# Kernel tuning notes

Hardware: AMD Instinct MI355X
Metric: run time of the kernel (lower is better)

Reference implementation:

```python
import jax, jax.numpy as jnp
import numpy as np

NUM_ITERATIONS = 3


def squash(s):
    # Faithful to the torch code: norm taken over dim=2 of (B,1,out_units,out_size,1),
    # i.e. over the out_units axis of (B, out_units, out_size).
    mag_sq = jnp.sum(s * s, axis=1, keepdims=True)  # (B,1,out_size)
    mag = jnp.sqrt(mag_sq)
    return mag_sq / (1.0 + mag_sq) * (s / mag)


def setup_inputs() -> dict:
    key = jax.random.key(0)
    k1, k2 = jax.random.split(key)
    B, in_units, in_size = 256, 8, 1152
    out_units, out_size = 10, 16
    x = jax.random.normal(k1, (B, in_units, in_size), dtype=jnp.float32)
    W = jax.random.normal(k2, (1, in_size, out_units, out_size, in_units), dtype=jnp.float32)
    return {"x": x, "W": W}


def reference(x, W):
    B = x.shape[0]
    in_size, out_units, out_size, in_units = W.shape[1:]
    Wm = W[0]  # (in_size, out_units, out_size, in_units)
    # u_hat[b,i,j,d] = sum_u W[i,j,d,u] * x[b,u,i]
    u_hat = jnp.einsum("ijdu,bui->bijd", Wm, x)  # (B, in_size, out_units, out_size)

    b_ij = jnp.ones((in_size, out_units), dtype=x.dtype)
    v = None
    for _ in range(NUM_ITERATIONS):
        c_ij = jax.nn.softmax(b_ij, axis=0)  # softmax over in_size (dim=1 in torch)
        s_j = jnp.einsum("ij,bijd->bjd", c_ij, u_hat)  # (B, out_units, out_size)
        v = squash(s_j)
        # agreement, averaged over batch as in the torch code
        u_vj1 = jnp.einsum("bijd,bjd->ij", u_hat, v) / B
        b_ij = b_ij + u_vj1
    # torch returns v_j.squeeze(1) with trailing singleton: (B, out_units, out_size, 1)
    return v[..., None]
```

## Files before the change

### kernel.cpp

```cpp
#include <hip/hip_runtime.h>
#include <cstddef>

#define BB   256
#define UU   8
#define ISZ  1152
#define JJ   10
#define DD   16
#define JD   (JJ*DD)
#define K1   (UU*ISZ)
#define ICH  16
#define NIC  (ISZ/ICH)
#define NJH  5

typedef short v8s __attribute__((ext_vector_type(8)));
typedef float f4v __attribute__((ext_vector_type(4)));
typedef unsigned short ush;

__device__ __forceinline__ ush f2bf(float f) {
    unsigned int u = __float_as_uint(f);
    unsigned int r = (u + 0x7fffu + ((u >> 16) & 1u)) >> 16;
    return (ush)r;
}
__device__ __forceinline__ float bf2f(ush h) {
    return __uint_as_float(((unsigned int)h) << 16);
}

__global__ void prep_kernel(const float* __restrict__ x,
                            ush* __restrict__ xsh, ush* __restrict__ xsl,
                            ush* __restrict__ xth, ush* __restrict__ xtl,
                            float* __restrict__ b_ij) {
    __shared__ float buf[32][8][65];
    int it = blockIdx.x;
    int bt = blockIdx.y;
    int i0 = it * 64, b0 = bt * 32;
    int t = threadIdx.x, lane = t & 63, wv = t >> 6;

    int flat = bt * 18 + it;
    if (flat < 45) b_ij[flat * 256 + t] = 1.0f;

    for (int rep = 0; rep < 64; ++rep) {
        int row = rep * 4 + wv;
        int bl = row >> 3, u = row & 7;
        buf[bl][u][lane] = x[(size_t)(b0 + bl) * K1 + (size_t)u * ISZ + i0 + lane];
    }
    __syncthreads();
    {
        int bl = t >> 3, u = t & 7;
        for (int il = 0; il < 64; ++il) {
            float v = buf[bl][u][il];
            ush h = f2bf(v);
            size_t o = (size_t)(i0 + il) * 2048 + (size_t)(b0 + bl) * 8 + u;
            xsh[o] = h; xsl[o] = f2bf(v - bf2f(h));
        }
    }
    {
        int g = t >> 5, bl = t & 31;
        for (int pass = 0; pass < 64; ++pass) {
            int cu = pass * 8 + g;
            int u = cu >> 6, il = cu & 63;
            float v = buf[bl][u][il];
            ush h = f2bf(v);
            size_t o = (size_t)(u * ISZ + i0 + il) * BB + b0 + bl;
            xth[o] = h; xtl[o] = f2bf(v - bf2f(h));
        }
    }
}

__global__ __launch_bounds__(256, 2) void sgemm_fused(
        const ush* __restrict__ xsh, const ush* __restrict__ xsl,
        const float* __restrict__ W, const float* __restrict__ b_ij,
        float* __restrict__ s_part, int first) {
    int jh = blockIdx.x, ic = blockIdx.y;
    int j0 = jh * 2, i0 = ic * ICH;
    int t = threadIdx.x, lane = t & 63, wv = t >> 6;
    int col = lane & 15, q = lane >> 4;

    __shared__ __align__(16) ush bh_[2][16][136];
    __shared__ __align__(16) ush bl_[2][16][136];
    __shared__ float c_lds[2][ICH];
    __shared__ float redm[4], reds[4];

    if (first) {
        if (t < 2 * ICH) c_lds[t >> 4][t & 15] = 1.0f / 1152.0f;
    } else {
        for (int jj = 0; jj < 2; ++jj) {
            const float* bp = b_ij + (size_t)(j0 + jj) * ISZ;
            float m = -1e30f;
            for (int k = t; k < ISZ; k += 256) m = fmaxf(m, bp[k]);
#pragma unroll
            for (int off = 32; off; off >>= 1) m = fmaxf(m, __shfl_down(m, off, 64));
            if (lane == 0) redm[wv] = m;
            __syncthreads();
            m = fmaxf(fmaxf(redm[0], redm[1]), fmaxf(redm[2], redm[3]));
            float ss = 0.f;
            for (int k = t; k < ISZ; k += 256) ss += __expf(bp[k] - m);
#pragma unroll
            for (int off = 32; off; off >>= 1) ss += __shfl_down(ss, off, 64);
            if (lane == 0) reds[wv] = ss;
            __syncthreads();
            float inv = 1.f / (reds[0] + reds[1] + reds[2] + reds[3]);
            if (t < ICH) c_lds[jj][t] = __expf(bp[i0 + t] - m) * inv;
            __syncthreads();
        }
    }
    __syncthreads();

    for (int slot = t; slot < 512; slot += 256) {
        int jj = slot >> 8, rem = slot & 255, ii = rem >> 4, d = rem & 15;
        const float* wp = W + (size_t)(i0 + ii) * 1280 + (j0 + jj) * 128 + d * 8;
        float4 wa = *(const float4*)wp;
        float4 wb = *(const float4*)(wp + 4);
        float ci = c_lds[jj][ii];
        float vals[8] = { wa.x * ci, wa.y * ci, wa.z * ci, wa.w * ci,
                          wb.x * ci, wb.y * ci, wb.z * ci, wb.w * ci };
        v8s hv, lv;
#pragma unroll
        for (int u = 0; u < 8; ++u) {
            ush h = f2bf(vals[u]);
            hv[u] = (short)h;
            lv[u] = (short)f2bf(vals[u] - bf2f(h));
        }
        *(v8s*)&bh_[jj][d][ii * 8] = hv;
        *(v8s*)&bl_[jj][d][ii * 8] = lv;
    }
    __syncthreads();

    int m_base = wv * 64;
    f4v acc[4][2];
#pragma unroll
    for (int mm = 0; mm < 4; ++mm)
#pragma unroll
        for (int jj = 0; jj < 2; ++jj) acc[mm][jj] = (f4v){0.f, 0.f, 0.f, 0.f};

#pragma unroll
    for (int s = 0; s < 4; ++s) {
        v8s bh0 = *(const v8s*)&bh_[0][col][s * 32 + q * 8];
        v8s bl0 = *(const v8s*)&bl_[0][col][s * 32 + q * 8];
        v8s bh1 = *(const v8s*)&bh_[1][col][s * 32 + q * 8];
        v8s bl1 = *(const v8s*)&bl_[1][col][s * 32 + q * 8];
        size_t abase = (size_t)(i0 + s * 4 + q) * 2048;
#pragma unroll
        for (int mm = 0; mm < 4; ++mm) {
            size_t ao = abase + (size_t)(m_base + mm * 16 + col) * 8;
            v8s ah = *(const v8s*)(xsh + ao);
            v8s al = *(const v8s*)(xsl + ao);
            acc[mm][0] = __builtin_amdgcn_mfma_f32_16x16x32_bf16(ah, bh0, acc[mm][0], 0, 0, 0);
            acc[mm][0] = __builtin_amdgcn_mfma_f32_16x16x32_bf16(ah, bl0, acc[mm][0], 0, 0, 0);
            acc[mm][0] = __builtin_amdgcn_mfma_f32_16x16x32_bf16(al, bh0, acc[mm][0], 0, 0, 0);
            acc[mm][1] = __builtin_amdgcn_mfma_f32_16x16x32_bf16(ah, bh1, acc[mm][1], 0, 0, 0);
            acc[mm][1] = __builtin_amdgcn_mfma_f32_16x16x32_bf16(ah, bl1, acc[mm][1], 0, 0, 0);
            acc[mm][1] = __builtin_amdgcn_mfma_f32_16x16x32_bf16(al, bh1, acc[mm][1], 0, 0, 0);
        }
    }
#pragma unroll
    for (int mm = 0; mm < 4; ++mm)
#pragma unroll
        for (int jj = 0; jj < 2; ++jj)
#pragma unroll
            for (int r = 0; r < 4; ++r)
                s_part[((size_t)ic * BB + m_base + mm * 16 + q * 4 + r) * JD
                       + (j0 + jj) * DD + col] = acc[mm][jj][r];
}

__global__ void reduce_squash(const float* __restrict__ s_part, float* __restrict__ v,
                              ush* __restrict__ vth, ush* __restrict__ vtl) {
    int b = blockIdx.x, t = threadIdx.x;
    __shared__ float sm[JD];
    if (t < JD) {
        float s = 0.f;
#pragma unroll 8
        for (int p = 0; p < NIC; ++p) s += s_part[((size_t)p * BB + b) * JD + t];
        sm[t] = s;
    }
    __syncthreads();
    if (t < JD) {
        int d = t & 15;
        float msq = 0.f;
#pragma unroll
        for (int j = 0; j < JJ; ++j) { float xx = sm[j * DD + d]; msq += xx * xx; }
        float val = msq / (1.f + msq) * sm[t] * rsqrtf(msq);
        v[(size_t)b * JD + t] = val;
        ush h = f2bf(val);
        vth[(size_t)t * BB + b] = h;
        vtl[(size_t)t * BB + b] = f2bf(val - bf2f(h));
    }
}

__global__ __launch_bounds__(256) void mgemm_agree(
        const ush* __restrict__ Ah, const ush* __restrict__ Al,
        const ush* __restrict__ Bh, const ush* __restrict__ Bl,
        const float* __restrict__ W, float* __restrict__ b_ij) {
    int w = threadIdx.x >> 6, lane = threadIdx.x & 63;
    int wj = blockIdx.x * 4 + w;
    int mt = wj / 576, nt = wj % 576;
    int m0 = mt * 16, n0 = nt * 16;
    int col = lane & 15, q = lane >> 4;
    size_t aoff = (size_t)(m0 + col) * BB + q * 8;
    size_t boff = (size_t)(n0 + col) * BB + q * 8;
    f4v acc = {0.f, 0.f, 0.f, 0.f};
#pragma unroll
    for (int s = 0; s < BB / 32; ++s) {
        v8s ah = *(const v8s*)(Ah + aoff);
        v8s al = *(const v8s*)(Al + aoff);
        v8s bh = *(const v8s*)(Bh + boff);
        v8s bl = *(const v8s*)(Bl + boff);
        acc = __builtin_amdgcn_mfma_f32_16x16x32_bf16(ah, bh, acc, 0, 0, 0);
        acc = __builtin_amdgcn_mfma_f32_16x16x32_bf16(ah, bl, acc, 0, 0, 0);
        acc = __builtin_amdgcn_mfma_f32_16x16x32_bf16(al, bh, acc, 0, 0, 0);
        aoff += 32; boff += 32;
    }
    int u = nt / 72;
    int i = (nt % 72) * 16 + col;
    const float* Wp = W + (size_t)i * 1280 + mt * 128 + q * 32 + u;
    float p = Wp[0] * acc[0] + Wp[8] * acc[1] + Wp[16] * acc[2] + Wp[24] * acc[3];
    p += __shfl_xor(p, 16, 64);
    p += __shfl_xor(p, 32, 64);
    if (q == 0) atomicAdd(&b_ij[(size_t)mt * ISZ + i], p * (1.0f / 256.0f));
}

extern "C" void kernel_launch(void* const* d_in, const int* in_sizes, int n_in,
                              void* d_out, int out_size, void* d_ws, size_t ws_size,
                              hipStream_t stream) {
    const float* x = (const float*)d_in[0];
    const float* W = (const float*)d_in[1];
    float* v_out = (float*)d_out;

    float* b_ij   = (float*)d_ws;
    float* s_part = b_ij + ISZ * JJ;
    ush* xsh = (ush*)(s_part + (size_t)NIC * BB * JD);
    ush* xsl = xsh + (size_t)ISZ * 2048;
    ush* xth = xsl + (size_t)ISZ * 2048;
    ush* xtl = xth + (size_t)K1 * BB;
    ush* vth = xtl + (size_t)K1 * BB;
    ush* vtl = vth + (size_t)JD * BB;

    hipLaunchKernelGGL(prep_kernel, dim3(18, 8), dim3(256), 0, stream,
                       x, xsh, xsl, xth, xtl, b_ij);
    for (int it = 0; it < 3; ++it) {
        hipLaunchKernelGGL(sgemm_fused, dim3(NJH, NIC), dim3(256), 0, stream,
                           xsh, xsl, W, b_ij, s_part, it == 0 ? 1 : 0);
        hipLaunchKernelGGL(reduce_squash, dim3(BB), dim3(192), 0, stream,
                           s_part, v_out, vth, vtl);
        if (it < 2) {
            hipLaunchKernelGGL(mgemm_agree, dim3(1440), dim3(256), 0, stream,
                               vth, vtl, xth, xtl, W, b_ij);
        }
    }
}
```

Measured before the change: 187.2 us.

## Fuse all routing stages into one persistent kernel with software grid barriers

Replaces the eight separate launches (prep, three sgemm/squash rounds, two agreement GEMMs) with a single persistent kernel of 512 blocks. Stages are separated by a flag-based global barrier built on atomics. The goal is to remove per-launch overhead and the gaps between kernels. The costs are reduced parallelism in some stages (the agreement GEMM loops over jobs), spin-wait overhead at each barrier, and a deadlock risk if all 512 blocks are not co-resident.

```diff
diff --git a/kernel.cpp b/kernel.cpp
--- a/kernel.cpp
+++ b/kernel.cpp
@@ -10,7 +10,7 @@
 #define K1   (UU*ISZ)
 #define ICH  16
 #define NIC  (ISZ/ICH)
-#define NJH  5
+#define GRID 512
 
 typedef short v8s __attribute__((ext_vector_type(8)));
 typedef float f4v __attribute__((ext_vector_type(4)));
@@ -24,198 +24,227 @@
 __device__ __forceinline__ float bf2f(ush h) {
     return __uint_as_float(((unsigned int)h) << 16);
 }
-
-__global__ void prep_kernel(const float* __restrict__ x,
-                            ush* __restrict__ xsh, ush* __restrict__ xsl,
-                            ush* __restrict__ xth, ush* __restrict__ xtl,
-                            float* __restrict__ b_ij) {
-    __shared__ float buf[32][8][65];
-    int it = blockIdx.x;
-    int bt = blockIdx.y;
-    int i0 = it * 64, b0 = bt * 32;
-    int t = threadIdx.x, lane = t & 63, wv = t >> 6;
-
-    int flat = bt * 18 + it;
-    if (flat < 45) b_ij[flat * 256 + t] = 1.0f;
-
-    for (int rep = 0; rep < 64; ++rep) {
-        int row = rep * 4 + wv;
-        int bl = row >> 3, u = row & 7;
-        buf[bl][u][lane] = x[(size_t)(b0 + bl) * K1 + (size_t)u * ISZ + i0 + lane];
+__device__ __forceinline__ float aload(const float* p) {
+    return __hip_atomic_load(p, __ATOMIC_RELAXED, __HIP_MEMORY_SCOPE_AGENT);
+}
+
+__device__ __forceinline__ void gbar(int* flags, int* rel, int ep) {
+    __syncthreads();
+    if (threadIdx.x == 0)
+        __hip_atomic_store(&flags[blockIdx.x], ep, __ATOMIC_RELEASE, __HIP_MEMORY_SCOPE_AGENT);
+    if (blockIdx.x == 0) {
+        for (int i = threadIdx.x; i < GRID; i += 256)
+            while (__hip_atomic_load(&flags[i], __ATOMIC_ACQUIRE, __HIP_MEMORY_SCOPE_AGENT) < ep)
+                __builtin_amdgcn_s_sleep(2);
+        __syncthreads();
+        if (threadIdx.x == 0)
+            __hip_atomic_store(rel, ep, __ATOMIC_RELEASE, __HIP_MEMORY_SCOPE_AGENT);
     }
+    if (threadIdx.x == 0)
+        while (__hip_atomic_load(rel, __ATOMIC_ACQUIRE, __HIP_MEMORY_SCOPE_AGENT) < ep)
+            __builtin_amdgcn_s_sleep(8);
     __syncthreads();
-    {
-        int bl = t >> 3, u = t & 7;
-        for (int il = 0; il < 64; ++il) {
-            float v = buf[bl][u][il];
-            ush h = f2bf(v);
-            size_t o = (size_t)(i0 + il) * 2048 + (size_t)(b0 + bl) * 8 + u;
-            xsh[o] = h; xsl[o] = f2bf(v - bf2f(h));
-        }
-    }
-    {
-        int g = t >> 5, bl = t & 31;
-        for (int pass = 0; pass < 64; ++pass) {
-            int cu = pass * 8 + g;
-            int u = cu >> 6, il = cu & 63;
-            float v = buf[bl][u][il];
-            ush h = f2bf(v);
-            size_t o = (size_t)(u * ISZ + i0 + il) * BB + b0 + bl;
-            xth[o] = h; xtl[o] = f2bf(v - bf2f(h));
-        }
-    }
-}
-
-__global__ __launch_bounds__(256, 2) void sgemm_fused(
-        const ush* __restrict__ xsh, const ush* __restrict__ xsl,
-        const float* __restrict__ W, const float* __restrict__ b_ij,
-        float* __restrict__ s_part, int first) {
-    int jh = blockIdx.x, ic = blockIdx.y;
-    int j0 = jh * 2, i0 = ic * ICH;
+}
+
+union __align__(16) SMem {
+    float prep_buf[16][8][65];
+    struct {
+        ush bh[2][16][136];
+        ush bl[2][16][136];
+        float c[2][ICH];
+        float redm[4], reds[4];
+    } sg;
+    float sm[JD];
+};
+
+__global__ __launch_bounds__(256, 2) void capsule_persist(
+        const float* __restrict__ x, const float* __restrict__ W,
+        float* __restrict__ v_out, int* flags, int* rel,
+        float* __restrict__ b_ij, float* __restrict__ s_part,
+        ush* __restrict__ xsh, ush* __restrict__ xsl,
+        ush* __restrict__ xth, ush* __restrict__ xtl,
+        ush* __restrict__ vth, ush* __restrict__ vtl) {
+    __shared__ SMem smem;
+    int bid = blockIdx.x;
     int t = threadIdx.x, lane = t & 63, wv = t >> 6;
     int col = lane & 15, q = lane >> 4;
-
-    __shared__ __align__(16) ush bh_[2][16][136];
-    __shared__ __align__(16) ush bl_[2][16][136];
-    __shared__ float c_lds[2][ICH];
-    __shared__ float redm[4], reds[4];
-
-    if (first) {
-        if (t < 2 * ICH) c_lds[t >> 4][t & 15] = 1.0f / 1152.0f;
-    } else {
-        for (int jj = 0; jj < 2; ++jj) {
-            const float* bp = b_ij + (size_t)(j0 + jj) * ISZ;
-            float m = -1e30f;
-            for (int k = t; k < ISZ; k += 256) m = fmaxf(m, bp[k]);
-#pragma unroll
-            for (int off = 32; off; off >>= 1) m = fmaxf(m, __shfl_down(m, off, 64));
-            if (lane == 0) redm[wv] = m;
+    int ep = 0;
+
+    if (bid < 45) b_ij[bid * 256 + t] = 1.0f;
+    if (bid < 288) {
+        int itile = bid % 18, btile = bid / 18;
+        int i0 = itile * 64, b0 = btile * 16;
+        for (int rep = 0; rep < 32; ++rep) {
+            int row = rep * 4 + wv;
+            int bl = row >> 3, u = row & 7;
+            smem.prep_buf[bl][u][lane] =
+                x[(size_t)(b0 + bl) * K1 + (size_t)u * ISZ + i0 + lane];
+        }
+        __syncthreads();
+        {
+            int half = t >> 7, bl = (t & 127) >> 3, u = t & 7;
+            for (int il = half * 32; il < half * 32 + 32; ++il) {
+                float v = smem.prep_buf[bl][u][il];
+                ush h = f2bf(v);
+                size_t o = (size_t)(i0 + il) * 2048 + (size_t)(b0 + bl) * 8 + u;
+                xsh[o] = h; xsl[o] = f2bf(v - bf2f(h));
+            }
+        }
+        {
+            int bl = t & 15, r = t >> 4;
+            for (int pass = 0; pass < 32; ++pass) {
+                int row = pass * 16 + r;
+                int u = row >> 6, il = row & 63;
+                float v = smem.prep_buf[bl][u][il];
+                ush h = f2bf(v);
+                size_t o = (size_t)(u * ISZ + i0 + il) * BB + b0 + bl;
+                xth[o] = h; xtl[o] = f2bf(v - bf2f(h));
+            }
+        }
+    }
+    gbar(flags, rel, ++ep);
+
+    for (int it = 0; it < 3; ++it) {
+        if (bid < 360) {
+            int jh = bid % 5, ic = bid / 5;
+            int j0 = jh * 2, i0 = ic * ICH;
+
+            if (it == 0) {
+                if (t < 2 * ICH) smem.sg.c[t >> 4][t & 15] = 1.0f / 1152.0f;
+            } else {
+                for (int jj = 0; jj < 2; ++jj) {
+                    const float* bp = b_ij + (size_t)(j0 + jj) * ISZ;
+                    float m = -1e30f;
+                    for (int k = t; k < ISZ; k += 256) m = fmaxf(m, aload(bp + k));
+#pragma unroll
+                    for (int off = 32; off; off >>= 1) m = fmaxf(m, __shfl_down(m, off, 64));
+                    if (lane == 0) smem.sg.redm[wv] = m;
+                    __syncthreads();
+                    m = fmaxf(fmaxf(smem.sg.redm[0], smem.sg.redm[1]),
+                              fmaxf(smem.sg.redm[2], smem.sg.redm[3]));
+                    float ss = 0.f;
+                    for (int k = t; k < ISZ; k += 256) ss += __expf(aload(bp + k) - m);
+#pragma unroll
+                    for (int off = 32; off; off >>= 1) ss += __shfl_down(ss, off, 64);
+                    if (lane == 0) smem.sg.reds[wv] = ss;
+                    __syncthreads();
+                    float inv = 1.f / (smem.sg.reds[0] + smem.sg.reds[1]
+                                       + smem.sg.reds[2] + smem.sg.reds[3]);
+                    if (t < ICH) smem.sg.c[jj][t] = __expf(aload(bp + i0 + t) - m) * inv;
+                    __syncthreads();
+                }
+            }
             __syncthreads();
-            m = fmaxf(fmaxf(redm[0], redm[1]), fmaxf(redm[2], redm[3]));
-            float ss = 0.f;
-            for (int k = t; k < ISZ; k += 256) ss += __expf(bp[k] - m);
-#pragma unroll
-            for (int off = 32; off; off >>= 1) ss += __shfl_down(ss, off, 64);
-            if (lane == 0) reds[wv] = ss;
+
+            for (int slot = t; slot < 512; slot += 256) {
+                int jj = slot >> 8, rem = slot & 255, ii = rem >> 4, d = rem & 15;
+                const float* wp = W + (size_t)(i0 + ii) * 1280 + (j0 + jj) * 128 + d * 8;
+                float4 wa = *(const float4*)wp;
+                float4 wb = *(const float4*)(wp + 4);
+                float ci = smem.sg.c[jj][ii];
+                float vals[8] = { wa.x * ci, wa.y * ci, wa.z * ci, wa.w * ci,
+                                  wb.x * ci, wb.y * ci, wb.z * ci, wb.w * ci };
+                v8s hv, lv;
+#pragma unroll
+                for (int u = 0; u < 8; ++u) {
+                    ush h = f2bf(vals[u]);
+                    hv[u] = (short)h;
+                    lv[u] = (short)f2bf(vals[u] - bf2f(h));
+                }
+                *(v8s*)&smem.sg.bh[jj][d][ii * 8] = hv;
+                *(v8s*)&smem.sg.bl[jj][d][ii * 8] = lv;
+            }
             __syncthreads();
-            float inv = 1.f / (reds[0] + reds[1] + reds[2] + reds[3]);
-            if (t < ICH) c_lds[jj][t] = __expf(bp[i0 + t] - m) * inv;
+
+            int m_base = wv * 64;
+            f4v acc[4][2];
+#pragma unroll
+            for (int mm = 0; mm < 4; ++mm)
+#pragma unroll
+                for (int jj = 0; jj < 2; ++jj) acc[mm][jj] = (f4v){0.f, 0.f, 0.f, 0.f};
+#pragma unroll
+            for (int s = 0; s < 4; ++s) {
+                v8s bh0 = *(const v8s*)&smem.sg.bh[0][col][s * 32 + q * 8];
+                v8s bl0 = *(const v8s*)&smem.sg.bl[0][col][s * 32 + q * 8];
+                v8s bh1 = *(const v8s*)&smem.sg.bh[1][col][s * 32 + q * 8];
+                v8s bl1 = *(const v8s*)&smem.sg.bl[1][col][s * 32 + q * 8];
+                size_t abase = (size_t)(i0 + s * 4 + q) * 2048;
+#pragma unroll
+                for (int mm = 0; mm < 4; ++mm) {
+                    size_t ao = abase + (size_t)(m_base + mm * 16 + col) * 8;
+                    v8s ah = *(const v8s*)(xsh + ao);
+                    v8s al = *(const v8s*)(xsl + ao);
+                    acc[mm][0] = __builtin_amdgcn_mfma_f32_16x16x32_bf16(ah, bh0, acc[mm][0], 0, 0, 0);
+                    acc[mm][0] = __builtin_amdgcn_mfma_f32_16x16x32_bf16(ah, bl0, acc[mm][0], 0, 0, 0);
+                    acc[mm][0] = __builtin_amdgcn_mfma_f32_16x16x32_bf16(al, bh0, acc[mm][0], 0, 0, 0);
+                    acc[mm][1] = __builtin_amdgcn_mfma_f32_16x16x32_bf16(ah, bh1, acc[mm][1], 0, 0, 0);
+                    acc[mm][1] = __builtin_amdgcn_mfma_f32_16x16x32_bf16(ah, bl1, acc[mm][1], 0, 0, 0);
+                    acc[mm][1] = __builtin_amdgcn_mfma_f32_16x16x32_bf16(al, bh1, acc[mm][1], 0, 0, 0);
+                }
+            }
+#pragma unroll
+            for (int mm = 0; mm < 4; ++mm)
+#pragma unroll
+                for (int jj = 0; jj < 2; ++jj)
+#pragma unroll
+                    for (int r = 0; r < 4; ++r)
+                        s_part[((size_t)ic * BB + m_base + mm * 16 + q * 4 + r) * JD
+                               + (j0 + jj) * DD + col] = acc[mm][jj][r];
+        }
+        gbar(flags, rel, ++ep);
+
+        if (bid < BB) {
+            int b = bid;
+            if (t < JD) {
+                float s = 0.f;
+#pragma unroll 8
+                for (int p = 0; p < NIC; ++p) s += s_part[((size_t)p * BB + b) * JD + t];
+                smem.sm[t] = s;
+            }
             __syncthreads();
-        }
+            if (t < JD) {
+                int d = t & 15;
+                float msq = 0.f;
+#pragma unroll
+                for (int j = 0; j < JJ; ++j) { float xx = smem.sm[j * DD + d]; msq += xx * xx; }
+                float val = msq / (1.f + msq) * smem.sm[t] * rsqrtf(msq);
+                v_out[(size_t)b * JD + t] = val;
+                ush h = f2bf(val);
+                vth[(size_t)t * BB + b] = h;
+                vtl[(size_t)t * BB + b] = f2bf(val - bf2f(h));
+            }
+        }
+        if (it == 2) break;
+        gbar(flags, rel, ++ep);
+
+        for (int job = bid; job < 1440; job += GRID) {
+            int wj = job * 4 + wv;
+            int mt = wj / 576, nt = wj % 576;
+            int m0 = mt * 16, n0 = nt * 16;
+            size_t aoff = (size_t)(m0 + col) * BB + q * 8;
+            size_t boff = (size_t)(n0 + col) * BB + q * 8;
+            f4v acc = {0.f, 0.f, 0.f, 0.f};
+#pragma unroll
+            for (int s = 0; s < BB / 32; ++s) {
+                v8s ah = *(const v8s*)(vth + aoff);
+                v8s al = *(const v8s*)(vtl + aoff);
+                v8s bh = *(const v8s*)(xth + boff);
+                v8s bl = *(const v8s*)(xtl + boff);
+                acc = __builtin_amdgcn_mfma_f32_16x16x32_bf16(ah, bh, acc, 0, 0, 0);
+                acc = __builtin_amdgcn_mfma_f32_16x16x32_bf16(ah, bl, acc, 0, 0, 0);
+                acc = __builtin_amdgcn_mfma_f32_16x16x32_bf16(al, bh, acc, 0, 0, 0);
+                aoff += 32; boff += 32;
+            }
+            int u = nt / 72;
+            int i = (nt % 72) * 16 + col;
+            const float* Wp = W + (size_t)i * 1280 + mt * 128 + q * 32 + u;
+            float p = Wp[0] * acc[0] + Wp[8] * acc[1] + Wp[16] * acc[2] + Wp[24] * acc[3];
+            p += __shfl_xor(p, 16, 64);
+            p += __shfl_xor(p, 32, 64);
+            if (q == 0) atomicAdd(&b_ij[(size_t)mt * ISZ + i], p * (1.0f / 256.0f));
+        }
+        gbar(flags, rel, ++ep);
     }
-    __syncthreads();
-
-    for (int slot = t; slot < 512; slot += 256) {
-        int jj = slot >> 8, rem = slot & 255, ii = rem >> 4, d = rem & 15;
-        const float* wp = W + (size_t)(i0 + ii) * 1280 + (j0 + jj) * 128 + d * 8;
-        float4 wa = *(const float4*)wp;
-        float4 wb = *(const float4*)(wp + 4);
-        float ci = c_lds[jj][ii];
-        float vals[8] = { wa.x * ci, wa.y * ci, wa.z * ci, wa.w * ci,
-                          wb.x * ci, wb.y * ci, wb.z * ci, wb.w * ci };
-        v8s hv, lv;
-#pragma unroll
-        for (int u = 0; u < 8; ++u) {
-            ush h = f2bf(vals[u]);
-            hv[u] = (short)h;
-            lv[u] = (short)f2bf(vals[u] - bf2f(h));
-        }
-        *(v8s*)&bh_[jj][d][ii * 8] = hv;
-        *(v8s*)&bl_[jj][d][ii * 8] = lv;
-    }
-    __syncthreads();
-
-    int m_base = wv * 64;
-    f4v acc[4][2];
-#pragma unroll
-    for (int mm = 0; mm < 4; ++mm)
-#pragma unroll
-        for (int jj = 0; jj < 2; ++jj) acc[mm][jj] = (f4v){0.f, 0.f, 0.f, 0.f};
-
-#pragma unroll
-    for (int s = 0; s < 4; ++s) {
-        v8s bh0 = *(const v8s*)&bh_[0][col][s * 32 + q * 8];
-        v8s bl0 = *(const v8s*)&bl_[0][col][s * 32 + q * 8];
-        v8s bh1 = *(const v8s*)&bh_[1][col][s * 32 + q * 8];
-        v8s bl1 = *(const v8s*)&bl_[1][col][s * 32 + q * 8];
-        size_t abase = (size_t)(i0 + s * 4 + q) * 2048;
-#pragma unroll
-        for (int mm = 0; mm < 4; ++mm) {
-            size_t ao = abase + (size_t)(m_base + mm * 16 + col) * 8;
-            v8s ah = *(const v8s*)(xsh + ao);
-            v8s al = *(const v8s*)(xsl + ao);
-            acc[mm][0] = __builtin_amdgcn_mfma_f32_16x16x32_bf16(ah, bh0, acc[mm][0], 0, 0, 0);
-            acc[mm][0] = __builtin_amdgcn_mfma_f32_16x16x32_bf16(ah, bl0, acc[mm][0], 0, 0, 0);
-            acc[mm][0] = __builtin_amdgcn_mfma_f32_16x16x32_bf16(al, bh0, acc[mm][0], 0, 0, 0);
-            acc[mm][1] = __builtin_amdgcn_mfma_f32_16x16x32_bf16(ah, bh1, acc[mm][1], 0, 0, 0);
-            acc[mm][1] = __builtin_amdgcn_mfma_f32_16x16x32_bf16(ah, bl1, acc[mm][1], 0, 0, 0);
-            acc[mm][1] = __builtin_amdgcn_mfma_f32_16x16x32_bf16(al, bh1, acc[mm][1], 0, 0, 0);
-        }
-    }
-#pragma unroll
-    for (int mm = 0; mm < 4; ++mm)
-#pragma unroll
-        for (int jj = 0; jj < 2; ++jj)
-#pragma unroll
-            for (int r = 0; r < 4; ++r)
-                s_part[((size_t)ic * BB + m_base + mm * 16 + q * 4 + r) * JD
-                       + (j0 + jj) * DD + col] = acc[mm][jj][r];
-}
-
-__global__ void reduce_squash(const float* __restrict__ s_part, float* __restrict__ v,
-                              ush* __restrict__ vth, ush* __restrict__ vtl) {
-    int b = blockIdx.x, t = threadIdx.x;
-    __shared__ float sm[JD];
-    if (t < JD) {
-        float s = 0.f;
-#pragma unroll 8
-        for (int p = 0; p < NIC; ++p) s += s_part[((size_t)p * BB + b) * JD + t];
-        sm[t] = s;
-    }
-    __syncthreads();
-    if (t < JD) {
-        int d = t & 15;
-        float msq = 0.f;
-#pragma unroll
-        for (int j = 0; j < JJ; ++j) { float xx = sm[j * DD + d]; msq += xx * xx; }
-        float val = msq / (1.f + msq) * sm[t] * rsqrtf(msq);
-        v[(size_t)b * JD + t] = val;
-        ush h = f2bf(val);
-        vth[(size_t)t * BB + b] = h;
-        vtl[(size_t)t * BB + b] = f2bf(val - bf2f(h));
-    }
-}
-
-__global__ __launch_bounds__(256) void mgemm_agree(
-        const ush* __restrict__ Ah, const ush* __restrict__ Al,
-        const ush* __restrict__ Bh, const ush* __restrict__ Bl,
-        const float* __restrict__ W, float* __restrict__ b_ij) {
-    int w = threadIdx.x >> 6, lane = threadIdx.x & 63;
-    int wj = blockIdx.x * 4 + w;
-    int mt = wj / 576, nt = wj % 576;
-    int m0 = mt * 16, n0 = nt * 16;
-    int col = lane & 15, q = lane >> 4;
-    size_t aoff = (size_t)(m0 + col) * BB + q * 8;
-    size_t boff = (size_t)(n0 + col) * BB + q * 8;
-    f4v acc = {0.f, 0.f, 0.f, 0.f};
-#pragma unroll
-    for (int s = 0; s < BB / 32; ++s) {
-        v8s ah = *(const v8s*)(Ah + aoff);
-        v8s al = *(const v8s*)(Al + aoff);
-        v8s bh = *(const v8s*)(Bh + boff);
-        v8s bl = *(const v8s*)(Bl + boff);
-        acc = __builtin_amdgcn_mfma_f32_16x16x32_bf16(ah, bh, acc, 0, 0, 0);
-        acc = __builtin_amdgcn_mfma_f32_16x16x32_bf16(ah, bl, acc, 0, 0, 0);
-        acc = __builtin_amdgcn_mfma_f32_16x16x32_bf16(al, bh, acc, 0, 0, 0);
-        aoff += 32; boff += 32;
-    }
-    int u = nt / 72;
-    int i = (nt % 72) * 16 + col;
-    const float* Wp = W + (size_t)i * 1280 + mt * 128 + q * 32 + u;
-    float p = Wp[0] * acc[0] + Wp[8] * acc[1] + Wp[16] * acc[2] + Wp[24] * acc[3];
-    p += __shfl_xor(p, 16, 64);
-    p += __shfl_xor(p, 32, 64);
-    if (q == 0) atomicAdd(&b_ij[(size_t)mt * ISZ + i], p * (1.0f / 256.0f));
 }
 
 extern "C" void kernel_launch(void* const* d_in, const int* in_sizes, int n_in,
@@ -225,7 +254,9 @@
     const float* W = (const float*)d_in[1];
     float* v_out = (float*)d_out;
 
-    float* b_ij   = (float*)d_ws;
+    int*   flags  = (int*)d_ws;
+    int*   rel    = flags + GRID;
+    float* b_ij   = (float*)d_ws + 1024;
     float* s_part = b_ij + ISZ * JJ;
     ush* xsh = (ush*)(s_part + (size_t)NIC * BB * JD);
     ush* xsl = xsh + (size_t)ISZ * 2048;
@@ -234,16 +265,8 @@
     ush* vth = xtl + (size_t)K1 * BB;
     ush* vtl = vth + (size_t)JD * BB;
 
-    hipLaunchKernelGGL(prep_kernel, dim3(18, 8), dim3(256), 0, stream,
-                       x, xsh, xsl, xth, xtl, b_ij);
-    for (int it = 0; it < 3; ++it) {
-        hipLaunchKernelGGL(sgemm_fused, dim3(NJH, NIC), dim3(256), 0, stream,
-                           xsh, xsl, W, b_ij, s_part, it == 0 ? 1 : 0);
-        hipLaunchKernelGGL(reduce_squash, dim3(BB), dim3(192), 0, stream,
-                           s_part, v_out, vth, vtl);
-        if (it < 2) {
-            hipLaunchKernelGGL(mgemm_agree, dim3(1440), dim3(256), 0, stream,
-                               vth, vtl, xth, xtl, W, b_ij);
-        }
-    }
-}
+    hipMemsetAsync(flags, 0, 1024 * sizeof(int), stream);
+    hipLaunchKernelGGL(capsule_persist, dim3(GRID), dim3(256), 0, stream,
+                       x, W, v_out, flags, rel, b_ij, s_part,
+                       xsh, xsl, xth, xtl, vth, vtl);
+}
```

Measured after the change: 690.6 us. +268.8%, slower.

## Fuse squash into agreement GEMM and replace partial-sum reduction with atomics

Applied to the files above, without the earlier changes.

The s-GEMM now accumulates its partial sums directly into a transposed s buffer with atomicAdd, and each block covers 48 input capsules instead of 16, looping over three staged W chunks. This removes the separate reduce_squash pass and the large partial-sum buffer. A new fused kernel computes the squash scale per batch column, converts v to bf16 hi/lo in LDS, and runs the agreement GEMM for all output units, keeping the x tiles in registers. It also zeroes the next iteration's accumulator. The cost is more float atomics, fewer blocks in the s-GEMM, and more serial work per block in the fused kernel.

```diff
diff --git a/kernel.cpp b/kernel.cpp
--- a/kernel.cpp
+++ b/kernel.cpp
@@ -8,9 +8,8 @@
 #define DD   16
 #define JD   (JJ*DD)
 #define K1   (UU*ISZ)
-#define ICH  16
+#define ICH  48
 #define NIC  (ISZ/ICH)
-#define NJH  5
 
 typedef short v8s __attribute__((ext_vector_type(8)));
 typedef float f4v __attribute__((ext_vector_type(4)));
@@ -28,7 +27,7 @@
 __global__ void prep_kernel(const float* __restrict__ x,
                             ush* __restrict__ xsh, ush* __restrict__ xsl,
                             ush* __restrict__ xth, ush* __restrict__ xtl,
-                            float* __restrict__ b_ij) {
+                            float* __restrict__ b_ij, float* __restrict__ s_red1) {
     __shared__ float buf[32][8][65];
     int it = blockIdx.x;
     int bt = blockIdx.y;
@@ -37,6 +36,8 @@
 
     int flat = bt * 18 + it;
     if (flat < 45) b_ij[flat * 256 + t] = 1.0f;
+    else if (flat < 85)
+        ((float4*)s_red1)[(flat - 45) * 256 + t] = make_float4(0.f, 0.f, 0.f, 0.f);
 
     for (int rep = 0; rep < 64; ++rep) {
         int row = rep * 4 + wv;
@@ -66,10 +67,10 @@
     }
 }
 
-__global__ __launch_bounds__(256, 2) void sgemm_fused(
+__global__ __launch_bounds__(256, 2) void sgemm_atomic(
         const ush* __restrict__ xsh, const ush* __restrict__ xsl,
         const float* __restrict__ W, const float* __restrict__ b_ij,
-        float* __restrict__ s_part, int first) {
+        float* __restrict__ s_red, int first) {
     int jh = blockIdx.x, ic = blockIdx.y;
     int j0 = jh * 2, i0 = ic * ICH;
     int t = threadIdx.x, lane = t & 63, wv = t >> 6;
@@ -81,7 +82,7 @@
     __shared__ float redm[4], reds[4];
 
     if (first) {
-        if (t < 2 * ICH) c_lds[t >> 4][t & 15] = 1.0f / 1152.0f;
+        if (t < 2 * ICH) c_lds[t / ICH][t % ICH] = 1.0f / 1152.0f;
     } else {
         for (int jj = 0; jj < 2; ++jj) {
             const float* bp = b_ij + (size_t)(j0 + jj) * ISZ;
@@ -103,27 +104,6 @@
             __syncthreads();
         }
     }
-    __syncthreads();
-
-    for (int slot = t; slot < 512; slot += 256) {
-        int jj = slot >> 8, rem = slot & 255, ii = rem >> 4, d = rem & 15;
-        const float* wp = W + (size_t)(i0 + ii) * 1280 + (j0 + jj) * 128 + d * 8;
-        float4 wa = *(const float4*)wp;
-        float4 wb = *(const float4*)(wp + 4);
-        float ci = c_lds[jj][ii];
-        float vals[8] = { wa.x * ci, wa.y * ci, wa.z * ci, wa.w * ci,
-                          wb.x * ci, wb.y * ci, wb.z * ci, wb.w * ci };
-        v8s hv, lv;
-#pragma unroll
-        for (int u = 0; u < 8; ++u) {
-            ush h = f2bf(vals[u]);
-            hv[u] = (short)h;
-            lv[u] = (short)f2bf(vals[u] - bf2f(h));
-        }
-        *(v8s*)&bh_[jj][d][ii * 8] = hv;
-        *(v8s*)&bl_[jj][d][ii * 8] = lv;
-    }
-    __syncthreads();
 
     int m_base = wv * 64;
     f4v acc[4][2];
@@ -132,24 +112,47 @@
 #pragma unroll
         for (int jj = 0; jj < 2; ++jj) acc[mm][jj] = (f4v){0.f, 0.f, 0.f, 0.f};
 
-#pragma unroll
-    for (int s = 0; s < 4; ++s) {
-        v8s bh0 = *(const v8s*)&bh_[0][col][s * 32 + q * 8];
-        v8s bl0 = *(const v8s*)&bl_[0][col][s * 32 + q * 8];
-        v8s bh1 = *(const v8s*)&bh_[1][col][s * 32 + q * 8];
-        v8s bl1 = *(const v8s*)&bl_[1][col][s * 32 + q * 8];
-        size_t abase = (size_t)(i0 + s * 4 + q) * 2048;
-#pragma unroll
-        for (int mm = 0; mm < 4; ++mm) {
-            size_t ao = abase + (size_t)(m_base + mm * 16 + col) * 8;
-            v8s ah = *(const v8s*)(xsh + ao);
-            v8s al = *(const v8s*)(xsl + ao);
-            acc[mm][0] = __builtin_amdgcn_mfma_f32_16x16x32_bf16(ah, bh0, acc[mm][0], 0, 0, 0);
-            acc[mm][0] = __builtin_amdgcn_mfma_f32_16x16x32_bf16(ah, bl0, acc[mm][0], 0, 0, 0);
-            acc[mm][0] = __builtin_amdgcn_mfma_f32_16x16x32_bf16(al, bh0, acc[mm][0], 0, 0, 0);
-            acc[mm][1] = __builtin_amdgcn_mfma_f32_16x16x32_bf16(ah, bh1, acc[mm][1], 0, 0, 0);
-            acc[mm][1] = __builtin_amdgcn_mfma_f32_16x16x32_bf16(ah, bl1, acc[mm][1], 0, 0, 0);
-            acc[mm][1] = __builtin_amdgcn_mfma_f32_16x16x32_bf16(al, bh1, acc[mm][1], 0, 0, 0);
+    for (int sc = 0; sc < 3; ++sc) {
+        __syncthreads();
+        for (int slot = t; slot < 512; slot += 256) {
+            int jj = slot >> 8, rem = slot & 255, ii = rem >> 4, d = rem & 15;
+            int iG = i0 + sc * 16 + ii;
+            const float* wp = W + (size_t)iG * 1280 + (j0 + jj) * 128 + d * 8;
+            float4 wa = *(const float4*)wp;
+            float4 wb = *(const float4*)(wp + 4);
+            float ci = c_lds[jj][sc * 16 + ii];
+            float vals[8] = { wa.x * ci, wa.y * ci, wa.z * ci, wa.w * ci,
+                              wb.x * ci, wb.y * ci, wb.z * ci, wb.w * ci };
+            v8s hv, lv;
+#pragma unroll
+            for (int u = 0; u < 8; ++u) {
+                ush h = f2bf(vals[u]);
+                hv[u] = (short)h;
+                lv[u] = (short)f2bf(vals[u] - bf2f(h));
+            }
+            *(v8s*)&bh_[jj][d][ii * 8] = hv;
+            *(v8s*)&bl_[jj][d][ii * 8] = lv;
+        }
+        __syncthreads();
+#pragma unroll
+        for (int s = 0; s < 4; ++s) {
+            v8s bh0 = *(const v8s*)&bh_[0][col][s * 32 + q * 8];
+            v8s bl0 = *(const v8s*)&bl_[0][col][s * 32 + q * 8];
+            v8s bh1 = *(const v8s*)&bh_[1][col][s * 32 + q * 8];
+            v8s bl1 = *(const v8s*)&bl_[1][col][s * 32 + q * 8];
+            size_t abase = (size_t)(i0 + sc * 16 + s * 4 + q) * 2048;
+#pragma unroll
+            for (int mm = 0; mm < 4; ++mm) {
+                size_t ao = abase + (size_t)(m_base + mm * 16 + col) * 8;
+                v8s ah = *(const v8s*)(xsh + ao);
+                v8s al = *(const v8s*)(xsl + ao);
+                acc[mm][0] = __builtin_amdgcn_mfma_f32_16x16x32_bf16(ah, bh0, acc[mm][0], 0, 0, 0);
+                acc[mm][0] = __builtin_amdgcn_mfma_f32_16x16x32_bf16(ah, bl0, acc[mm][0], 0, 0, 0);
+                acc[mm][0] = __builtin_amdgcn_mfma_f32_16x16x32_bf16(al, bh0, acc[mm][0], 0, 0, 0);
+                acc[mm][1] = __builtin_amdgcn_mfma_f32_16x16x32_bf16(ah, bh1, acc[mm][1], 0, 0, 0);
+                acc[mm][1] = __builtin_amdgcn_mfma_f32_16x16x32_bf16(ah, bl1, acc[mm][1], 0, 0, 0);
+                acc[mm][1] = __builtin_amdgcn_mfma_f32_16x16x32_bf16(al, bh1, acc[mm][1], 0, 0, 0);
+            }
         }
     }
 #pragma unroll
@@ -158,64 +161,90 @@
         for (int jj = 0; jj < 2; ++jj)
 #pragma unroll
             for (int r = 0; r < 4; ++r)
-                s_part[((size_t)ic * BB + m_base + mm * 16 + q * 4 + r) * JD
-                       + (j0 + jj) * DD + col] = acc[mm][jj][r];
-}
-
-__global__ void reduce_squash(const float* __restrict__ s_part, float* __restrict__ v,
-                              ush* __restrict__ vth, ush* __restrict__ vtl) {
+                atomicAdd(&s_red[(size_t)((j0 + jj) * DD + col) * BB
+                                 + m_base + mm * 16 + q * 4 + r], acc[mm][jj][r]);
+}
+
+__global__ __launch_bounds__(256, 2) void sqmg_kernel(
+        const ush* __restrict__ xth, const ush* __restrict__ xtl,
+        const float* __restrict__ s_red, const float* __restrict__ W,
+        float* __restrict__ b_ij, float* __restrict__ s_red_next) {
+    int bid = blockIdx.x;
+    int t = threadIdx.x, lane = t & 63, wv = t >> 6;
+    int col = lane & 15, q = lane >> 4;
+
+    if (bid < 40)
+        ((float4*)s_red_next)[bid * 256 + t] = make_float4(0.f, 0.f, 0.f, 0.f);
+
+    int nt = bid * 4 + wv;
+    int n0 = nt * 16;
+
+    v8s Bh[8], Bl[8];
+#pragma unroll
+    for (int s = 0; s < 8; ++s) {
+        size_t bo = (size_t)(n0 + col) * BB + s * 32 + q * 8;
+        Bh[s] = *(const v8s*)(xth + bo);
+        Bl[s] = *(const v8s*)(xtl + bo);
+    }
+
+    float msq[16];
+#pragma unroll
+    for (int d = 0; d < 16; ++d) msq[d] = 0.f;
+#pragma unroll 16
+    for (int jd = 0; jd < JD; ++jd) {
+        float val = s_red[(size_t)jd * BB + t];
+        msq[jd & 15] += val * val;
+    }
+    float g[16];
+#pragma unroll
+    for (int d = 0; d < 16; ++d)
+        g[d] = msq[d] / (1.f + msq[d]) * rsqrtf(msq[d]);
+
+    __shared__ __align__(16) ush avh[16][264];
+    __shared__ __align__(16) ush avl[16][264];
+
+    int u = nt / 72;
+    int i = (nt % 72) * 16 + col;
+
+    for (int mt = 0; mt < JJ; ++mt) {
+        __syncthreads();
+#pragma unroll
+        for (int d = 0; d < 16; ++d) {
+            float val = s_red[(size_t)(mt * DD + d) * BB + t] * g[d];
+            ush h = f2bf(val);
+            avh[d][t] = h;
+            avl[d][t] = f2bf(val - bf2f(h));
+        }
+        __syncthreads();
+        f4v acc = {0.f, 0.f, 0.f, 0.f};
+#pragma unroll
+        for (int s = 0; s < 8; ++s) {
+            v8s ah = *(const v8s*)&avh[col][s * 32 + q * 8];
+            v8s al = *(const v8s*)&avl[col][s * 32 + q * 8];
+            acc = __builtin_amdgcn_mfma_f32_16x16x32_bf16(ah, Bh[s], acc, 0, 0, 0);
+            acc = __builtin_amdgcn_mfma_f32_16x16x32_bf16(ah, Bl[s], acc, 0, 0, 0);
+            acc = __builtin_amdgcn_mfma_f32_16x16x32_bf16(al, Bh[s], acc, 0, 0, 0);
+        }
+        const float* Wp = W + (size_t)i * 1280 + mt * 128 + q * 32 + u;
+        float p = Wp[0] * acc[0] + Wp[8] * acc[1] + Wp[16] * acc[2] + Wp[24] * acc[3];
+        p += __shfl_xor(p, 16, 64);
+        p += __shfl_xor(p, 32, 64);
+        if (q == 0) atomicAdd(&b_ij[(size_t)mt * ISZ + i], p * (1.0f / 256.0f));
+    }
+}
+
+__global__ void squash_out(const float* __restrict__ s_red, float* __restrict__ v) {
     int b = blockIdx.x, t = threadIdx.x;
     __shared__ float sm[JD];
-    if (t < JD) {
-        float s = 0.f;
-#pragma unroll 8
-        for (int p = 0; p < NIC; ++p) s += s_part[((size_t)p * BB + b) * JD + t];
-        sm[t] = s;
-    }
+    if (t < JD) sm[t] = s_red[(size_t)t * BB + b];
     __syncthreads();
     if (t < JD) {
         int d = t & 15;
         float msq = 0.f;
 #pragma unroll
         for (int j = 0; j < JJ; ++j) { float xx = sm[j * DD + d]; msq += xx * xx; }
-        float val = msq / (1.f + msq) * sm[t] * rsqrtf(msq);
-        v[(size_t)b * JD + t] = val;
-        ush h = f2bf(val);
-        vth[(size_t)t * BB + b] = h;
-        vtl[(size_t)t * BB + b] = f2bf(val - bf2f(h));
-    }
-}
-
-__global__ __launch_bounds__(256) void mgemm_agree(
-        const ush* __restrict__ Ah, const ush* __restrict__ Al,
-        const ush* __restrict__ Bh, const ush* __restrict__ Bl,
-        const float* __restrict__ W, float* __restrict__ b_ij) {
-    int w = threadIdx.x >> 6, lane = threadIdx.x & 63;
-    int wj = blockIdx.x * 4 + w;
-    int mt = wj / 576, nt = wj % 576;
-    int m0 = mt * 16, n0 = nt * 16;
-    int col = lane & 15, q = lane >> 4;
-    size_t aoff = (size_t)(m0 + col) * BB + q * 8;
-    size_t boff = (size_t)(n0 + col) * BB + q * 8;
-    f4v acc = {0.f, 0.f, 0.f, 0.f};
-#pragma unroll
-    for (int s = 0; s < BB / 32; ++s) {
-        v8s ah = *(const v8s*)(Ah + aoff);
-        v8s al = *(const v8s*)(Al + aoff);
-        v8s bh = *(const v8s*)(Bh + boff);
-        v8s bl = *(const v8s*)(Bl + boff);
-        acc = __builtin_amdgcn_mfma_f32_16x16x32_bf16(ah, bh, acc, 0, 0, 0);
-        acc = __builtin_amdgcn_mfma_f32_16x16x32_bf16(ah, bl, acc, 0, 0, 0);
-        acc = __builtin_amdgcn_mfma_f32_16x16x32_bf16(al, bh, acc, 0, 0, 0);
-        aoff += 32; boff += 32;
-    }
-    int u = nt / 72;
-    int i = (nt % 72) * 16 + col;
-    const float* Wp = W + (size_t)i * 1280 + mt * 128 + q * 32 + u;
-    float p = Wp[0] * acc[0] + Wp[8] * acc[1] + Wp[16] * acc[2] + Wp[24] * acc[3];
-    p += __shfl_xor(p, 16, 64);
-    p += __shfl_xor(p, 32, 64);
-    if (q == 0) atomicAdd(&b_ij[(size_t)mt * ISZ + i], p * (1.0f / 256.0f));
+        v[(size_t)b * JD + t] = msq / (1.f + msq) * sm[t] * rsqrtf(msq);
+    }
 }
 
 extern "C" void kernel_launch(void* const* d_in, const int* in_sizes, int n_in,
@@ -225,25 +254,26 @@
     const float* W = (const float*)d_in[1];
     float* v_out = (float*)d_out;
 
-    float* b_ij   = (float*)d_ws;
-    float* s_part = b_ij + ISZ * JJ;
-    ush* xsh = (ush*)(s_part + (size_t)NIC * BB * JD);
+    float* b_ij = (float*)d_ws;
+    float* s1   = b_ij + ISZ * JJ;
+    float* s2   = s1 + JD * BB;
+    float* s3   = s2 + JD * BB;
+    ush* xsh = (ush*)(s3 + JD * BB);
     ush* xsl = xsh + (size_t)ISZ * 2048;
     ush* xth = xsl + (size_t)ISZ * 2048;
     ush* xtl = xth + (size_t)K1 * BB;
-    ush* vth = xtl + (size_t)K1 * BB;
-    ush* vtl = vth + (size_t)JD * BB;
 
     hipLaunchKernelGGL(prep_kernel, dim3(18, 8), dim3(256), 0, stream,
-                       x, xsh, xsl, xth, xtl, b_ij);
-    for (int it = 0; it < 3; ++it) {
-        hipLaunchKernelGGL(sgemm_fused, dim3(NJH, NIC), dim3(256), 0, stream,
-                           xsh, xsl, W, b_ij, s_part, it == 0 ? 1 : 0);
-        hipLaunchKernelGGL(reduce_squash, dim3(BB), dim3(192), 0, stream,
-                           s_part, v_out, vth, vtl);
-        if (it < 2) {
-            hipLaunchKernelGGL(mgemm_agree, dim3(1440), dim3(256), 0, stream,
-                               vth, vtl, xth, xtl, W, b_ij);
-        }
-    }
-}
+                       x, xsh, xsl, xth, xtl, b_ij, s1);
+    hipLaunchKernelGGL(sgemm_atomic, dim3(5, NIC), dim3(256), 0, stream,
+                       xsh, xsl, W, b_ij, s1, 1);
+    hipLaunchKernelGGL(sqmg_kernel, dim3(144), dim3(256), 0, stream,
+                       xth, xtl, s1, W, b_ij, s2);
+    hipLaunchKernelGGL(sgemm_atomic, dim3(5, NIC), dim3(256), 0, stream,
+                       xsh, xsl, W, b_ij, s2, 0);
+    hipLaunchKernelGGL(sqmg_kernel, dim3(144), dim3(256), 0, stream,
+                       xth, xtl, s2, W, b_ij, s3);
+    hipLaunchKernelGGL(sgemm_atomic, dim3(5, NIC), dim3(256), 0, stream,
+                       xsh, xsl, W, b_ij, s3, 0);
+    hipLaunchKernelGGL(squash_out, dim3(BB), dim3(192), 0, stream, s3, v_out);
+}
```

Result: slower. 236.3 us (+26.2%).
